# Optimization experiments

Hardware: AMD Instinct MI355X
Metric: run time of the kernel (lower is better)

## Reference

```python
import jax, jax.numpy as jnp
import numpy as np

B, S, H = 1, 2048, 4096
NH, NKV, HD = 32, 8, 128
GROUP = 128
NEG = jnp.float32(-1e9)


def setup_inputs() -> dict:
    key = jax.random.key(0)
    ks = jax.random.split(key, 13)
    inp = {"hidden_states": jax.random.normal(ks[0], (B, S, H), dtype=jnp.float32)}

    def qparams(k1, k2, k3, out_dim, in_dim):
        qw = jax.random.randint(k1, (out_dim, in_dim), 0, 16, dtype=jnp.int32)
        sc = jax.random.uniform(k2, (out_dim, in_dim // GROUP), dtype=jnp.float32) * 0.02 + 0.001
        zp = jax.random.randint(k3, (out_dim, in_dim // GROUP), 0, 16, dtype=jnp.int32)
        return qw, sc, zp

    inp["q_qw"], inp["q_sc"], inp["q_zp"] = qparams(ks[1], ks[2], ks[3], NH * HD, H)
    inp["k_qw"], inp["k_sc"], inp["k_zp"] = qparams(ks[4], ks[5], ks[6], NKV * HD, H)
    inp["v_qw"], inp["v_sc"], inp["v_zp"] = qparams(ks[7], ks[8], ks[9], NKV * HD, H)
    inp["o_qw"], inp["o_sc"], inp["o_zp"] = qparams(ks[10], ks[11], ks[12], NH * HD, H)
    return inp


def dequant(qw, sc, zp):
    # W4A16 groupwise dequant: w = (q - zero_point) * scale, group along input dim
    out_dim, in_dim = qw.shape
    g = in_dim // sc.shape[1]
    w = (qw.reshape(out_dim, -1, g) - zp[:, :, None]).astype(jnp.float32) * sc[:, :, None]
    return w.reshape(out_dim, in_dim)


def reference(hidden_states, q_qw, q_sc, q_zp, k_qw, k_sc, k_zp,
              v_qw, v_sc, v_zp, o_qw, o_sc, o_zp):
    x = hidden_states  # [B, S, H]
    grp = NH // NKV  # GQA groups = 4

    q = jnp.einsum('bsh,oh->bso', x, dequant(q_qw, q_sc, q_zp))
    k = jnp.einsum('bsh,oh->bso', x, dequant(k_qw, k_sc, k_zp))
    v = jnp.einsum('bsh,oh->bso', x, dequant(v_qw, v_sc, v_zp))

    # [B, NKV, grp, S, HD] for q; [B, NKV, S, HD] for k, v (avoid repeat_kv materialization)
    q = q.reshape(B, S, NKV, grp, HD).transpose(0, 2, 3, 1, 4)
    k = k.reshape(B, S, NKV, HD).transpose(0, 2, 1, 3)
    v = v.reshape(B, S, NKV, HD).transpose(0, 2, 1, 3)

    scale = 1.0 / jnp.sqrt(jnp.float32(HD))
    scores = jnp.einsum('bngqd,bnkd->bngqk', q, k) * scale  # [B,NKV,grp,S,S]
    causal = jnp.tril(jnp.ones((S, S), dtype=bool))
    scores = jnp.where(causal[None, None, None], scores, NEG)
    probs = jax.nn.softmax(scores, axis=-1)
    attn = jnp.einsum('bngqk,bnkd->bngqd', probs, v)  # [B,NKV,grp,S,HD]

    attn = attn.transpose(0, 3, 1, 2, 4).reshape(B, S, NH * HD)
    out = jnp.einsum('bso,ho->bsh', attn, dequant(o_qw, o_sc, o_zp).T.T) if False else jnp.einsum('bsf,of->bso', attn, dequant(o_qw, o_sc, o_zp))
    return out
```

## Files before the change

### kernel.cpp

```cpp
#include <hip/hip_runtime.h>
#include <stdint.h>

#define DI __device__ __forceinline__

typedef __attribute__((ext_vector_type(8))) _Float16 f16x8;
typedef __attribute__((ext_vector_type(4))) float f32x4;
typedef __attribute__((ext_vector_type(4))) int   i32x4;
typedef __attribute__((ext_vector_type(4))) float fvec4;
typedef __attribute__((ext_vector_type(8))) unsigned short u16x8;
typedef __attribute__((ext_vector_type(4))) unsigned short u16x4;

constexpr int S2   = 2048;
constexpr int NHD  = 4096;
constexpr int KVD  = 1024;
constexpr int QKVW = 6144;
constexpr float SCALE_LOG2E = 0.08838834764831845f * 1.4426950408889634f;

DI unsigned short f32_f16(float f) {
    union { _Float16 h; unsigned short u; } v;
    v.h = (_Float16)f;
    return v.u;
}

DI f32x4 mfma16(f16x8 a, f16x8 b, f32x4 c) {
    return __builtin_amdgcn_mfma_f32_16x16x32_f16(a, b, c, 0, 0, 0);
}

DI void load_lds16(const void* g, void* l) {
    __builtin_amdgcn_global_load_lds(
        (const __attribute__((address_space(1))) void*)(uintptr_t)g,
        (__attribute__((address_space(3))) void*)(uintptr_t)l, 16, 0, 0);
}

__global__ __launch_bounds__(256) void k_cast(const float* __restrict__ in,
                                              unsigned short* __restrict__ out) {
    int i = (blockIdx.x * 256 + threadIdx.x) * 4;
    fvec4 v = *(const fvec4*)(in + i);
    u16x4 o;
#pragma unroll
    for (int j = 0; j < 4; ++j) o[j] = f32_f16(v[j]);
    *(u16x4*)(out + i) = o;
}

__global__ __launch_bounds__(256) void k_prep(const int* __restrict__ qw,
                                              const float* __restrict__ sc,
                                              const int* __restrict__ zp,
                                              unsigned short* __restrict__ outW) {
    long long t = (long long)blockIdx.x * 256 + threadIdx.x;
    long long base = t * 8;
    int n = (int)(base >> 12);
    int g = (int)((base >> 7) & 31);
    float s = sc[n * 32 + g];
    int   z = zp[n * 32 + g];
    i32x4 a = *(const i32x4*)(qw + base);
    i32x4 b = *(const i32x4*)(qw + base + 4);
    u16x8 o;
#pragma unroll
    for (int j = 0; j < 4; ++j) {
        o[j]     = f32_f16((float)(a[j] - z) * s);
        o[4 + j] = f32_f16((float)(b[j] - z) * s);
    }
    *(u16x8*)(outW + base) = o;
}

template <typename CT>
__global__ __launch_bounds__(256) void k_gemm(const unsigned short* __restrict__ A,
                                              const unsigned short* __restrict__ B,
                                              CT* __restrict__ C, int N) {
    constexpr int K = 4096;
    constexpr int NT = K / 32;
    __shared__ __align__(16) unsigned short Al[2][128 * 32];
    __shared__ __align__(16) unsigned short Bl[2][128 * 32];
    const int m0 = blockIdx.y * 128, n0 = blockIdx.x * 128;
    const int tid = threadIdx.x;
    const int wave = tid >> 6, lane = tid & 63;
    const int wm = wave >> 1, wn = wave & 1;
    const int lq = lane & 15, lg = lane >> 4;
    const int srow = lane >> 2;
    const int scol = (((lane & 3) ^ ((srow >> 1) & 3)) << 3);
    const int cx   = ((lg ^ ((lq >> 1) & 3)) << 3);
    f32x4 acc[4][4] = {};

    auto stage = [&](int k0, int b) {
#pragma unroll
        for (int it = 0; it < 2; ++it) {
            const int r0 = (wave * 2 + it) * 16;
            load_lds16(A + (long long)(m0 + r0 + srow) * K + k0 + scol, &Al[b][r0 * 32]);
            load_lds16(B + (long long)(n0 + r0 + srow) * K + k0 + scol, &Bl[b][r0 * 32]);
        }
    };

    stage(0, 0);
    int buf = 0;
    for (int t = 0; t < NT; ++t) {
        if (t + 1 < NT) {
            stage((t + 1) * 32, buf ^ 1);
            asm volatile("s_waitcnt vmcnt(4)" ::: "memory");
        } else {
            asm volatile("s_waitcnt vmcnt(0)" ::: "memory");
        }
        __builtin_amdgcn_s_barrier();
        __builtin_amdgcn_sched_barrier(0);
        f16x8 af[4], bf[4];
#pragma unroll
        for (int i = 0; i < 4; ++i) {
            af[i] = *(const f16x8*)(&Al[buf][(wm * 64 + i * 16 + lq) * 32 + cx]);
            bf[i] = *(const f16x8*)(&Bl[buf][(wn * 64 + i * 16 + lq) * 32 + cx]);
        }
        __builtin_amdgcn_s_setprio(1);
#pragma unroll
        for (int mi = 0; mi < 4; ++mi)
#pragma unroll
            for (int ni = 0; ni < 4; ++ni)
                acc[mi][ni] = mfma16(af[mi], bf[ni], acc[mi][ni]);
        __builtin_amdgcn_s_setprio(0);
        __builtin_amdgcn_sched_barrier(0);
        __builtin_amdgcn_s_barrier();
        __builtin_amdgcn_sched_barrier(0);
        buf ^= 1;
    }
#pragma unroll
    for (int mi = 0; mi < 4; ++mi)
#pragma unroll
        for (int ni = 0; ni < 4; ++ni)
#pragma unroll
            for (int r = 0; r < 4; ++r) {
                const int row = m0 + wm * 64 + mi * 16 + lg * 4 + r;
                const int col = n0 + wn * 64 + ni * 16 + lq;
                const float v = acc[mi][ni][r];
                if constexpr (sizeof(CT) == 2) C[(long long)row * N + col] = (CT)f32_f16(v);
                else                           C[(long long)row * N + col] = v;
            }
}

__global__ __launch_bounds__(256) void k_transpose_v(const unsigned short* __restrict__ QKV,
                                                     unsigned short* __restrict__ VT) {
    __shared__ unsigned short tile[32][33];
    const int s0 = blockIdx.x * 32, d0 = blockIdx.y * 32, hk = blockIdx.z;
    const int tx = threadIdx.x & 31, ty = threadIdx.x >> 5;
#pragma unroll
    for (int j = 0; j < 4; ++j)
        tile[ty + j * 8][tx] =
            QKV[(long long)(s0 + ty + j * 8) * QKVW + (NHD + KVD) + hk * 128 + d0 + tx];
    __syncthreads();
#pragma unroll
    for (int j = 0; j < 4; ++j)
        VT[((long long)hk * 128 + d0 + ty + j * 8) * S2 + s0 + tx] = tile[tx][ty + j * 8];
}

__global__ __launch_bounds__(256, 4) void k_attn(const unsigned short* __restrict__ QKV,
                                                 const unsigned short* __restrict__ VT,
                                                 unsigned short* __restrict__ O) {
    __shared__ __align__(16) unsigned short Ks[2][32 * 128];
    __shared__ __align__(16) unsigned short Vs[2][128 * 32];
    __shared__ __align__(16) unsigned short Ps[4][16 * 40];
    const int bid = blockIdx.x;
    const int hkv = bid & 7;
    const int tq  = bid >> 3;
    const int g   = (tq < 64) ? tq : 191 - tq;
    const int nt  = (g >> 1) + 1;
    const int q0  = g * 16;
    const int tid = threadIdx.x;
    const int w = tid >> 6, lane = tid & 63;
    const int lq = lane & 15, lg = lane >> 4;
    const int h = hkv * 4 + w;

    const unsigned short* Kg  = QKV + NHD + hkv * 128;
    const unsigned short* VTg = VT + (long long)hkv * 128 * S2;

    const int ksr = lane >> 4;
    const int ksc = lane & 15;
    const int vsr = lane >> 2;
    const int vsc = lane & 3;
    const int vsx = (lane >> 3) & 3;

    f16x8 qf[4];
    const unsigned short* qp = QKV + (long long)(q0 + lq) * QKVW + h * 128;
#pragma unroll
    for (int kc = 0; kc < 4; ++kc) qf[kc] = *(const f16x8*)(qp + kc * 32 + lg * 8);

    f32x4 oacc[8] = {};
    float m[4], l[4];
#pragma unroll
    for (int r = 0; r < 4; ++r) { m[r] = -1e30f; l[r] = 0.f; }

    auto stage = [&](int j0, int b) {
#pragma unroll
        for (int i = 0; i < 2; ++i) {
            const int r = 8 * w + 4 * i + ksr;
            load_lds16(Kg + (long long)(j0 + r) * QKVW + ((ksc ^ (r & 7)) << 3),
                       &Ks[b][(8 * w + 4 * i) * 128]);
        }
#pragma unroll
        for (int i = 0; i < 2; ++i) {
            const int r = 32 * w + 16 * i + vsr;
            load_lds16(VTg + (long long)r * S2 + j0 + ((vsc ^ vsx) << 3),
                       &Vs[b][(32 * w + 16 * i) * 32]);
        }
    };

    stage(0, 0);
    int buf = 0;
    for (int t = 0; t < nt; ++t) {
        const int j0 = t * 32;
        __syncthreads();
        if (t + 1 < nt) stage(j0 + 32, buf ^ 1);

        f32x4 sv[2] = {};
        __builtin_amdgcn_s_setprio(1);
#pragma unroll
        for (int kc = 0; kc < 4; ++kc)
#pragma unroll
            for (int jj = 0; jj < 2; ++jj) {
                const int c = (kc * 4 + lg) ^ (lq & 7);
                f16x8 kf = *(const f16x8*)&Ks[buf][(jj * 16 + lq) * 128 + c * 8];
                sv[jj] = mfma16(qf[kc], kf, sv[jj]);
            }
        __builtin_amdgcn_s_setprio(0);

        float t0a[4], t1a[4], pl[4];
        const bool diag = (t == nt - 1);
#pragma unroll
        for (int r = 0; r < 4; ++r) {
            float t0 = sv[0][r] * SCALE_LOG2E;
            float t1 = sv[1][r] * SCALE_LOG2E;
            if (diag) {
                const int qg = q0 + lg * 4 + r;
                if (j0 + lq > qg)      t0 = -INFINITY;
                if (j0 + 16 + lq > qg) t1 = -INFINITY;
            }
            t0a[r] = t0; t1a[r] = t1;
            pl[r] = fmaxf(t0, t1);
        }
        const bool grow = (pl[0] > m[0] + 8.f) || (pl[1] > m[1] + 8.f) ||
                          (pl[2] > m[2] + 8.f) || (pl[3] > m[3] + 8.f);
        if (__any(grow)) {
#pragma unroll
            for (int r = 0; r < 4; ++r) {
                float mx = pl[r];
                mx = fmaxf(mx, __shfl_xor(mx, 1));
                mx = fmaxf(mx, __shfl_xor(mx, 2));
                mx = fmaxf(mx, __shfl_xor(mx, 4));
                mx = fmaxf(mx, __shfl_xor(mx, 8));
                const float mn = fmaxf(m[r], mx);
                const float alpha = exp2f(m[r] - mn);
                m[r] = mn;
                l[r] *= alpha;
#pragma unroll
                for (int nb = 0; nb < 8; ++nb) oacc[nb][r] *= alpha;
            }
        }
#pragma unroll
        for (int r = 0; r < 4; ++r) {
            const float p0 = exp2f(t0a[r] - m[r]);
            const float p1 = exp2f(t1a[r] - m[r]);
            l[r] += p0 + p1;
            Ps[w][(lg * 4 + r) * 40 + lq]      = f32_f16(p0);
            Ps[w][(lg * 4 + r) * 40 + 16 + lq] = f32_f16(p1);
        }
        const f16x8 pf = *(const f16x8*)&Ps[w][lq * 40 + lg * 8];
        __builtin_amdgcn_s_setprio(1);
#pragma unroll
        for (int nb = 0; nb < 8; ++nb) {
            const int c = lg ^ ((lq >> 1) & 3);
            f16x8 vf = *(const f16x8*)&Vs[buf][(nb * 16 + lq) * 32 + c * 8];
            oacc[nb] = mfma16(pf, vf, oacc[nb]);
        }
        __builtin_amdgcn_s_setprio(0);
        buf ^= 1;
    }

    float linv[4];
#pragma unroll
    for (int r = 0; r < 4; ++r) {
        float s = l[r];
        s += __shfl_xor(s, 1);
        s += __shfl_xor(s, 2);
        s += __shfl_xor(s, 4);
        s += __shfl_xor(s, 8);
        linv[r] = 1.0f / s;
    }
#pragma unroll
    for (int nb = 0; nb < 8; ++nb)
#pragma unroll
        for (int r = 0; r < 4; ++r) {
            const int row = q0 + lg * 4 + r;
            const int col = h * 128 + nb * 16 + lq;
            O[(long long)row * NHD + col] = f32_f16(oacc[nb][r] * linv[r]);
        }
}

extern "C" void kernel_launch(void* const* d_in, const int* in_sizes, int n_in,
                              void* d_out, int out_size, void* d_ws, size_t ws_size,
                              hipStream_t stream) {
    (void)in_sizes; (void)n_in; (void)out_size; (void)ws_size;
    const float* hs  = (const float*)d_in[0];
    const int*   qqw = (const int*)d_in[1];
    const float* qsc = (const float*)d_in[2];
    const int*   qzp = (const int*)d_in[3];
    const int*   kqw = (const int*)d_in[4];
    const float* ksc = (const float*)d_in[5];
    const int*   kzp = (const int*)d_in[6];
    const int*   vqw = (const int*)d_in[7];
    const float* vsc = (const float*)d_in[8];
    const int*   vzp = (const int*)d_in[9];
    const int*   oqw = (const int*)d_in[10];
    const float* osc = (const float*)d_in[11];
    const int*   ozp = (const int*)d_in[12];

    char* ws = (char*)d_ws;
    unsigned short* x16  = (unsigned short*)(ws);
    unsigned short* wbuf = (unsigned short*)(ws + (16ULL << 20));
    unsigned short* vt   = (unsigned short*)(ws + (65ULL << 20));
    unsigned short* xatt = (unsigned short*)(ws + (69ULL << 20));
    unsigned short* qkv  = (unsigned short*)d_out;
    float* out = (float*)d_out;

    k_cast<<<8192, 256, 0, stream>>>(hs, x16);
    k_prep<<<8192, 256, 0, stream>>>(qqw, qsc, qzp, wbuf);
    k_prep<<<2048, 256, 0, stream>>>(kqw, ksc, kzp, wbuf + (size_t)4096 * 4096);
    k_prep<<<2048, 256, 0, stream>>>(vqw, vsc, vzp, wbuf + (size_t)5120 * 4096);
    k_gemm<unsigned short><<<dim3(48, 16), 256, 0, stream>>>(x16, wbuf, qkv, QKVW);
    k_transpose_v<<<dim3(64, 4, 8), 256, 0, stream>>>(qkv, vt);
    k_prep<<<8192, 256, 0, stream>>>(oqw, osc, ozp, wbuf);
    k_attn<<<1024, 256, 0, stream>>>(qkv, vt, xatt);
    k_gemm<float><<<dim3(32, 16), 256, 0, stream>>>(xatt, wbuf, out, 4096);
}
```

Baseline: 342.5 us.

## Use 8-wave 256-row GEMM tiles with triple-buffered LDS and XCD-aware block remap

Replaces the 128x128 four-wave GEMM with a 512-thread kernel using 256-row tiles (256x256 for QKV, 256x128 for the output projection). LDS goes from two to three buffers, so each iteration needs one barrier instead of two, and each block is remapped so neighbouring tiles land on the same XCD for better L2 reuse. The aims are higher arithmetic intensity per LDS load and less synchronisation. In exchange it uses more registers (up to 128 accumulator floats per lane) and more LDS, and launches fewer blocks (192 and 256), which may underfill the GPU's compute units.

```diff
diff --git a/kernel.cpp b/kernel.cpp
--- a/kernel.cpp
+++ b/kernel.cpp
@@ -63,70 +63,83 @@
     *(u16x8*)(outW + base) = o;
 }
 
-template <typename CT>
-__global__ __launch_bounds__(256) void k_gemm(const unsigned short* __restrict__ A,
-                                              const unsigned short* __restrict__ B,
-                                              CT* __restrict__ C, int N) {
-    constexpr int K = 4096;
-    constexpr int NT = K / 32;
-    __shared__ __align__(16) unsigned short Al[2][128 * 32];
-    __shared__ __align__(16) unsigned short Bl[2][128 * 32];
-    const int m0 = blockIdx.y * 128, n0 = blockIdx.x * 128;
+template <typename CT, int NREP>
+__global__ __launch_bounds__(512) void k_gemm8(const unsigned short* __restrict__ A,
+                                               const unsigned short* __restrict__ B,
+                                               CT* __restrict__ C, int N) {
+    constexpr int K = 4096, BK = 32, NT = K / BK;
+    constexpr int BN = NREP * 64;
+    __shared__ __align__(16) unsigned short Al[3][256 * 32];
+    __shared__ __align__(16) unsigned short Bl[3][BN * 32];
+    const int nbx = N / BN;
+    const int tot = nbx * (int)gridDim.y;
+    const int h   = (int)blockIdx.x + (int)blockIdx.y * nbx;
+    const int lid = (h & 7) * (tot >> 3) + (h >> 3);
+    const int m0 = (lid / nbx) * 256, n0 = (lid % nbx) * BN;
     const int tid = threadIdx.x;
-    const int wave = tid >> 6, lane = tid & 63;
-    const int wm = wave >> 1, wn = wave & 1;
+    const int w = tid >> 6, lane = tid & 63;
+    const int wm = w >> 2, wn = w & 3;
     const int lq = lane & 15, lg = lane >> 4;
+    const int cx = (lg ^ ((lq >> 1) & 3)) << 3;
     const int srow = lane >> 2;
-    const int scol = (((lane & 3) ^ ((srow >> 1) & 3)) << 3);
-    const int cx   = ((lg ^ ((lq >> 1) & 3)) << 3);
-    f32x4 acc[4][4] = {};
-
-    auto stage = [&](int k0, int b) {
-#pragma unroll
-        for (int it = 0; it < 2; ++it) {
-            const int r0 = (wave * 2 + it) * 16;
-            load_lds16(A + (long long)(m0 + r0 + srow) * K + k0 + scol, &Al[b][r0 * 32]);
-            load_lds16(B + (long long)(n0 + r0 + srow) * K + k0 + scol, &Bl[b][r0 * 32]);
+    const int gc = (((lane & 3) ^ ((lane >> 3) & 3)) << 3);
+    f32x4 acc[8][NREP] = {};
+
+    auto stage = [&](int k0, int sl) {
+#pragma unroll
+        for (int j = 0; j < 2; ++j)
+            load_lds16(A + (long long)(m0 + (j * 8 + w) * 16 + srow) * K + k0 + gc,
+                       &Al[sl][(j * 8 + w) * 512]);
+        if constexpr (NREP == 4) {
+#pragma unroll
+            for (int j = 0; j < 2; ++j)
+                load_lds16(B + (long long)(n0 + (j * 8 + w) * 16 + srow) * K + k0 + gc,
+                           &Bl[sl][(j * 8 + w) * 512]);
+        } else {
+            load_lds16(B + (long long)(n0 + w * 16 + srow) * K + k0 + gc,
+                       &Bl[sl][w * 512]);
         }
     };
 
     stage(0, 0);
-    int buf = 0;
-    for (int t = 0; t < NT; ++t) {
-        if (t + 1 < NT) {
-            stage((t + 1) * 32, buf ^ 1);
-            asm volatile("s_waitcnt vmcnt(4)" ::: "memory");
+    stage(BK, 1);
+    int cs = 0, ss = 2;
+    for (int kt = 0; kt < NT; ++kt) {
+        if (kt < NT - 1) {
+            if constexpr (NREP == 4) asm volatile("s_waitcnt vmcnt(4)" ::: "memory");
+            else                     asm volatile("s_waitcnt vmcnt(3)" ::: "memory");
         } else {
             asm volatile("s_waitcnt vmcnt(0)" ::: "memory");
         }
         __builtin_amdgcn_s_barrier();
         __builtin_amdgcn_sched_barrier(0);
-        f16x8 af[4], bf[4];
-#pragma unroll
-        for (int i = 0; i < 4; ++i) {
-            af[i] = *(const f16x8*)(&Al[buf][(wm * 64 + i * 16 + lq) * 32 + cx]);
-            bf[i] = *(const f16x8*)(&Bl[buf][(wn * 64 + i * 16 + lq) * 32 + cx]);
-        }
+        if (kt + 2 < NT) stage((kt + 2) * BK, ss);
+        f16x8 af[8], bf[NREP];
+#pragma unroll
+        for (int i = 0; i < 8; ++i)
+            af[i] = *(const f16x8*)(&Al[cs][(wm * 128 + i * 16 + lq) * 32 + cx]);
+#pragma unroll
+        for (int i = 0; i < NREP; ++i)
+            bf[i] = *(const f16x8*)(&Bl[cs][(wn * (NREP * 16) + i * 16 + lq) * 32 + cx]);
         __builtin_amdgcn_s_setprio(1);
 #pragma unroll
-        for (int mi = 0; mi < 4; ++mi)
-#pragma unroll
-            for (int ni = 0; ni < 4; ++ni)
+        for (int mi = 0; mi < 8; ++mi)
+#pragma unroll
+            for (int ni = 0; ni < NREP; ++ni)
                 acc[mi][ni] = mfma16(af[mi], bf[ni], acc[mi][ni]);
         __builtin_amdgcn_s_setprio(0);
         __builtin_amdgcn_sched_barrier(0);
-        __builtin_amdgcn_s_barrier();
-        __builtin_amdgcn_sched_barrier(0);
-        buf ^= 1;
+        if (++cs == 3) cs = 0;
+        if (++ss == 3) ss = 0;
     }
 #pragma unroll
-    for (int mi = 0; mi < 4; ++mi)
-#pragma unroll
-        for (int ni = 0; ni < 4; ++ni)
+    for (int mi = 0; mi < 8; ++mi)
+#pragma unroll
+        for (int ni = 0; ni < NREP; ++ni)
 #pragma unroll
             for (int r = 0; r < 4; ++r) {
-                const int row = m0 + wm * 64 + mi * 16 + lg * 4 + r;
-                const int col = n0 + wn * 64 + ni * 16 + lq;
+                const int row = m0 + wm * 128 + mi * 16 + lg * 4 + r;
+                const int col = n0 + wn * (NREP * 16) + ni * 16 + lq;
                 const float v = acc[mi][ni][r];
                 if constexpr (sizeof(CT) == 2) C[(long long)row * N + col] = (CT)f32_f16(v);
                 else                           C[(long long)row * N + col] = v;
@@ -320,9 +333,9 @@
     k_prep<<<8192, 256, 0, stream>>>(qqw, qsc, qzp, wbuf);
     k_prep<<<2048, 256, 0, stream>>>(kqw, ksc, kzp, wbuf + (size_t)4096 * 4096);
     k_prep<<<2048, 256, 0, stream>>>(vqw, vsc, vzp, wbuf + (size_t)5120 * 4096);
-    k_gemm<unsigned short><<<dim3(48, 16), 256, 0, stream>>>(x16, wbuf, qkv, QKVW);
+    k_gemm8<unsigned short, 4><<<dim3(24, 8), 512, 0, stream>>>(x16, wbuf, qkv, QKVW);
     k_transpose_v<<<dim3(64, 4, 8), 256, 0, stream>>>(qkv, vt);
     k_prep<<<8192, 256, 0, stream>>>(oqw, osc, ozp, wbuf);
     k_attn<<<1024, 256, 0, stream>>>(qkv, vt, xatt);
-    k_gemm<float><<<dim3(32, 16), 256, 0, stream>>>(xatt, wbuf, out, 4096);
-}
+    k_gemm8<float, 2><<<dim3(32, 8), 512, 0, stream>>>(xatt, wbuf, out, 4096);
+}
```

Measured after the change: 319.3 us. -6.8%, faster.
